# Kernel tuning notes

Hardware: AMD Instinct MI355X
Metric: run time of the kernel (lower is better)

The kernel has to match this reference:

```python
import jax, jax.numpy as jnp
import numpy as np

N_EMBD = 1024
N_HEAD = 16


def setup_inputs() -> dict:
    key = jax.random.key(0)
    ks = jax.random.split(key, 5)
    C = N_EMBD
    x = jax.random.normal(ks[0], (4, 2048, C), dtype=jnp.float32)
    s = 1.0 / np.sqrt(C)
    W_attn = jax.random.normal(ks[1], (C, 3 * C), dtype=jnp.float32) * s
    b_attn = jnp.zeros((3 * C,), dtype=jnp.float32)
    W_proj = jax.random.normal(ks[2], (C, C), dtype=jnp.float32) * s
    b_proj = jnp.zeros((C,), dtype=jnp.float32)
    return {"x": x, "W_attn": W_attn, "b_attn": b_attn, "W_proj": W_proj, "b_proj": b_proj}


def reference(x, W_attn, b_attn, W_proj, b_proj):
    B, T, C = x.shape
    H = N_HEAD
    D = C // H
    qkv = x @ W_attn + b_attn                      # [B,T,3C]
    q, k, v = jnp.split(qkv, 3, axis=-1)
    # [B,H,T,D]
    q = q.reshape(B, T, H, D).transpose(0, 2, 1, 3)
    k = k.reshape(B, T, H, D).transpose(0, 2, 1, 3)
    v = v.reshape(B, T, H, D).transpose(0, 2, 1, 3)
    scale = 1.0 / jnp.sqrt(jnp.asarray(D, dtype=x.dtype))
    att = jnp.einsum('bhqd,bhkd->bhqk', q, k) * scale   # [B,H,T,T]
    causal = jnp.tril(jnp.ones((T, T), dtype=bool))
    att = jnp.where(causal, att, jnp.finfo(att.dtype).min)
    att = jax.nn.softmax(att, axis=-1)
    y = jnp.einsum('bhqk,bhkd->bhqd', att, v)            # [B,H,T,D]
    y = y.transpose(0, 2, 1, 3).reshape(B, T, C)
    return y @ W_proj + b_proj
```

## Files before the change

### kernel.cpp

```cpp
#include <hip/hip_runtime.h>
#include <type_traits>

typedef __attribute__((ext_vector_type(8))) short short8;
typedef __attribute__((ext_vector_type(8))) unsigned short ushort8;
typedef __attribute__((ext_vector_type(4))) float floatx4;

__device__ __forceinline__ unsigned short f2bf(float f) {
    union { float f; unsigned int i; } v;
    v.f = f;
    unsigned int u = v.i;
    unsigned int r = (u + 0x7FFFu + ((u >> 16) & 1u)) >> 16;
    return (unsigned short)r;
}

__device__ __forceinline__ void gload_lds16(const unsigned short* g, unsigned short* lds_base) {
    __builtin_amdgcn_global_load_lds(
        (const __attribute__((address_space(1))) unsigned int*)g,
        (__attribute__((address_space(3))) unsigned int*)lds_base,
        16, 0, 0);
}

__global__ __launch_bounds__(256) void cvt_f32_bf16_kernel(
    const float* __restrict__ src, unsigned short* __restrict__ dst, int n8)
{
    int i = blockIdx.x * 256 + threadIdx.x;
    if (i >= n8) return;
    const float4* s = (const float4*)src + (size_t)i * 2;
    float4 a = s[0];
    float4 b = s[1];
    ushort8 r;
    r[0] = f2bf(a.x); r[1] = f2bf(a.y); r[2] = f2bf(a.z); r[3] = f2bf(a.w);
    r[4] = f2bf(b.x); r[5] = f2bf(b.y); r[6] = f2bf(b.z); r[7] = f2bf(b.w);
    *((ushort8*)dst + i) = r;
}

__global__ __launch_bounds__(256) void transpose_cvt_kernel(
    const float* __restrict__ src, unsigned short* __restrict__ dst, int K, int N)
{
    __shared__ float tile[32][33];
    const int tx = threadIdx.x & 31;
    const int ty = threadIdx.x >> 5;
    const int k0 = blockIdx.y * 32, n0 = blockIdx.x * 32;
#pragma unroll
    for (int i = 0; i < 4; ++i)
        tile[ty + i * 8][tx] = src[(size_t)(k0 + ty + i * 8) * N + n0 + tx];
    __syncthreads();
#pragma unroll
    for (int i = 0; i < 4; ++i)
        dst[(size_t)(n0 + ty + i * 8) * K + k0 + tx] = f2bf(tile[tx][ty + i * 8]);
}

template <int MODE, typename OutT>
__global__ __launch_bounds__(256) void gemm128_kernel(
    const unsigned short* __restrict__ A,
    const unsigned short* __restrict__ Bt,
    const float* __restrict__ bias,
    OutT* __restrict__ C,
    unsigned short* __restrict__ Qo,
    unsigned short* __restrict__ Ko,
    unsigned short* __restrict__ Vto,
    int M, int N, int K)
{
    __shared__ __align__(16) unsigned short As[128 * 32];
    __shared__ __align__(16) unsigned short Bs[128 * 32];

    const int tid  = threadIdx.x;
    const int lane = tid & 63;
    const int w    = tid >> 6;
    const int wm   = w & 1;
    const int wn   = w >> 1;
    const int quad = lane >> 4;
    const int l16  = lane & 15;

    const int m0 = blockIdx.y * 128;
    const int n0 = blockIdx.x * 128;

    floatx4 acc[4][4];
#pragma unroll
    for (int i = 0; i < 4; ++i)
#pragma unroll
        for (int j = 0; j < 4; ++j) acc[i][j] = (floatx4)0.0f;

    const int r0 = tid >> 2;
    const int kc = (tid & 3) << 3;
    const unsigned short* Ag = A  + (size_t)(m0 + r0) * K + kc;
    const unsigned short* Bg = Bt + (size_t)(n0 + r0) * K + kc;
    unsigned short* AsW = As + w * 512;
    unsigned short* BsW = Bs + w * 512;

    for (int k0 = 0; k0 < K; k0 += 32) {
        __syncthreads();
#pragma unroll
        for (int i = 0; i < 2; ++i) {
            gload_lds16(Ag + (size_t)(i * 64) * K + k0, AsW + i * 2048);
            gload_lds16(Bg + (size_t)(i * 64) * K + k0, BsW + i * 2048);
        }
        __syncthreads();

        short8 a[4], b[4];
#pragma unroll
        for (int mi = 0; mi < 4; ++mi)
            a[mi] = *(const short8*)&As[(wm * 64 + mi * 16 + l16) * 32 + (quad << 3)];
#pragma unroll
        for (int ni = 0; ni < 4; ++ni)
            b[ni] = *(const short8*)&Bs[(wn * 64 + ni * 16 + l16) * 32 + (quad << 3)];
#pragma unroll
        for (int mi = 0; mi < 4; ++mi)
#pragma unroll
            for (int ni = 0; ni < 4; ++ni)
                acc[mi][ni] = __builtin_amdgcn_mfma_f32_16x16x32_bf16(a[mi], b[ni], acc[mi][ni], 0, 0, 0);
    }

#pragma unroll
    for (int ni = 0; ni < 4; ++ni) {
        const int n = n0 + wn * 64 + ni * 16 + l16;
        const float bval = bias[n];
#pragma unroll
        for (int mi = 0; mi < 4; ++mi) {
#pragma unroll
            for (int r = 0; r < 4; ++r) {
                const int m = m0 + wm * 64 + mi * 16 + (quad << 2) + r;
                const float val = acc[mi][ni][r] + bval;
                if constexpr (MODE == 0) {
                    if constexpr (std::is_same<OutT, unsigned short>::value)
                        C[(size_t)m * N + n] = f2bf(val);
                    else
                        C[(size_t)m * N + n] = val;
                } else {
                    const int seg = n >> 10;
                    const int nl  = n & 1023;
                    if (seg == 0) {
                        Qo[(size_t)m * 1024 + nl] = f2bf(val);
                    } else if (seg == 1) {
                        Ko[(size_t)m * 1024 + nl] = f2bf(val);
                    } else {
                        const int bb = m >> 11, t = m & 2047;
                        Vto[((size_t)bb * 1024 + nl) * 2048 + t] = f2bf(val);
                    }
                }
            }
        }
    }
}

__global__ __launch_bounds__(256) void attn_kernel(
    const unsigned short* __restrict__ Q,
    const unsigned short* __restrict__ Kq,
    const unsigned short* __restrict__ Vt,
    unsigned short* __restrict__ Y)
{
    const int T = 2048;

    int idx = blockIdx.x;
    int qt  = 31 - (idx >> 6);
    int bh  = idx & 63;
    int b   = bh >> 4;
    int h   = bh & 15;

    const int tid  = threadIdx.x;
    const int lane = tid & 63;
    const int w    = tid >> 6;
    const int quad = lane >> 4;
    const int l16  = lane & 15;

    __shared__ __align__(16) unsigned short Ks[32][72];
    __shared__ __align__(16) unsigned short Vs[64 * 32];
    __shared__ __align__(16) unsigned short Ps[4][16][40];

    const unsigned short* qp =
        Q + (size_t)(b * T + qt * 64 + (w << 4) + l16) * 1024 + h * 64;
    short8 qf0 = *(const short8*)(qp + (quad << 3));
    short8 qf1 = *(const short8*)(qp + 32 + (quad << 3));

    float l_i[4];
    floatx4 o[4];
#pragma unroll
    for (int r = 0; r < 4; ++r) l_i[r] = 0.0f;
#pragma unroll
    for (int ns = 0; ns < 4; ++ns) o[ns] = (floatx4)0.0f;

    const int srow = tid >> 3;
    const int scol = (tid & 7) << 3;
    const int vrow = tid >> 2;
    const int vcol = (tid & 3) << 3;
    const unsigned short* vbase = Vt + ((size_t)(b * 1024 + h * 64 + vrow)) * 2048 + vcol;
    const int qrow  = qt * 64 + (w << 4) + (quad << 2);
    const int wrow0 = qt * 64 + (w << 4);

    const float SC = 0.125f;
    const float MB = -12.0f;

    const int ktiles = 2 * qt + 2;
    for (int kt = 0; kt < ktiles; ++kt) {
        const int key0 = kt << 5;
        __syncthreads();
        const unsigned short* kp =
            Kq + (size_t)(b * T + key0 + srow) * 1024 + h * 64 + scol;
        *(int4*)&Ks[srow][scol] = *(const int4*)kp;
        gload_lds16(vbase + key0, Vs + w * 512);
        __syncthreads();

        floatx4 s0 = (floatx4)0.0f, s1 = (floatx4)0.0f;
        {
            short8 kf00 = *(const short8*)&Ks[l16][quad << 3];
            short8 kf01 = *(const short8*)&Ks[l16][32 + (quad << 3)];
            short8 kf10 = *(const short8*)&Ks[16 + l16][quad << 3];
            short8 kf11 = *(const short8*)&Ks[16 + l16][32 + (quad << 3)];
            s0 = __builtin_amdgcn_mfma_f32_16x16x32_bf16(qf0, kf00, s0, 0, 0, 0);
            s0 = __builtin_amdgcn_mfma_f32_16x16x32_bf16(qf1, kf01, s0, 0, 0, 0);
            s1 = __builtin_amdgcn_mfma_f32_16x16x32_bf16(qf0, kf10, s1, 0, 0, 0);
            s1 = __builtin_amdgcn_mfma_f32_16x16x32_bf16(qf1, kf11, s1, 0, 0, 0);
        }

        if (key0 + 31 <= wrow0) {
#pragma unroll
            for (int r = 0; r < 4; ++r) {
                float p0 = __expf(fmaf(s0[r], SC, MB));
                float p1 = __expf(fmaf(s1[r], SC, MB));
                l_i[r] += p0 + p1;
                Ps[w][(quad << 2) + r][l16]      = f2bf(p0);
                Ps[w][(quad << 2) + r][16 + l16] = f2bf(p1);
            }
        } else {
            const int kg0 = key0 + l16;
#pragma unroll
            for (int r = 0; r < 4; ++r) {
                float a0 = (kg0      <= qrow + r) ? fmaf(s0[r], SC, MB) : -1e5f;
                float a1 = (kg0 + 16 <= qrow + r) ? fmaf(s1[r], SC, MB) : -1e5f;
                float p0 = __expf(a0);
                float p1 = __expf(a1);
                l_i[r] += p0 + p1;
                Ps[w][(quad << 2) + r][l16]      = f2bf(p0);
                Ps[w][(quad << 2) + r][16 + l16] = f2bf(p1);
            }
        }

        short8 pf = *(const short8*)&Ps[w][l16][quad << 3];
#pragma unroll
        for (int ns = 0; ns < 4; ++ns) {
            short8 vf = *(const short8*)&Vs[((ns << 4) + l16) * 32 + (quad << 3)];
            o[ns] = __builtin_amdgcn_mfma_f32_16x16x32_bf16(pf, vf, o[ns], 0, 0, 0);
        }
    }

#pragma unroll
    for (int r = 0; r < 4; ++r) {
        float s = l_i[r];
        s += __shfl_xor(s, 1, 64);
        s += __shfl_xor(s, 2, 64);
        s += __shfl_xor(s, 4, 64);
        s += __shfl_xor(s, 8, 64);
        l_i[r] = 1.0f / s;
    }

#pragma unroll
    for (int ns = 0; ns < 4; ++ns) {
        int d = (ns << 4) + l16;
#pragma unroll
        for (int r = 0; r < 4; ++r) {
            int t = qt * 64 + (w << 4) + (quad << 2) + r;
            Y[(size_t)(b * T + t) * 1024 + h * 64 + d] = f2bf(o[ns][r] * l_i[r]);
        }
    }
}

extern "C" void kernel_launch(void* const* d_in, const int* in_sizes, int n_in,
                              void* d_out, int out_size, void* d_ws, size_t ws_size,
                              hipStream_t stream) {
    const float* x  = (const float*)d_in[0];
    const float* Wa = (const float*)d_in[1];
    const float* ba = (const float*)d_in[2];
    const float* Wp = (const float*)d_in[3];
    const float* bp = (const float*)d_in[4];
    float* out = (float*)d_out;

    const size_t NX = (size_t)8192 * 1024;

    unsigned short* Qb  = (unsigned short*)d_ws;
    unsigned short* Kb  = Qb  + NX;
    unsigned short* Vtb = Kb  + NX;
    unsigned short* Yb  = Vtb + NX;
    unsigned short* xb  = Yb  + NX;
    unsigned short* Wat = xb  + NX;
    unsigned short* Wpt = Wat + (size_t)3072 * 1024;

    cvt_f32_bf16_kernel<<<(int)(NX / 8 / 256), 256, 0, stream>>>(x, xb, (int)(NX / 8));
    transpose_cvt_kernel<<<dim3(3072 / 32, 1024 / 32), 256, 0, stream>>>(Wa, Wat, 1024, 3072);
    transpose_cvt_kernel<<<dim3(1024 / 32, 1024 / 32), 256, 0, stream>>>(Wp, Wpt, 1024, 1024);

    gemm128_kernel<1, unsigned short><<<dim3(3072 / 128, 8192 / 128), 256, 0, stream>>>(
        xb, Wat, ba, (unsigned short*)nullptr, Qb, Kb, Vtb, 8192, 3072, 1024);

    attn_kernel<<<4 * 16 * (2048 / 64), 256, 0, stream>>>(Qb, Kb, Vtb, Yb);

    gemm128_kernel<0, float><<<dim3(1024 / 128, 8192 / 128), 256, 0, stream>>>(
        Yb, Wpt, bp, out, nullptr, nullptr, nullptr, 8192, 1024, 1024);
}
```

Measured before the change: 293.5 us.

## Widen attention key tiles to 64 with direct-to-LDS K/V loads; vectorize V^T stores

The attention kernel now processes 64 keys per iteration instead of 32. That halves the loop trips and barrier pairs and doubles the MFMA work per synchronization. K and V tiles are both loaded with global_load_lds into a k-chunk-major LDS layout, replacing register-staged K stores. The QKV GEMM epilogue writes the transposed V as packed 4-element 8-byte stores instead of scattered 2-byte stores. The costs are more LDS and registers per block and coarser causal masking on the diagonal tile.

Measured after the change: 276.0 us. 6.0% less time.

```diff
diff --git a/kernel.cpp b/kernel.cpp
--- a/kernel.cpp
+++ b/kernel.cpp
@@ -115,28 +115,37 @@
     for (int ni = 0; ni < 4; ++ni) {
         const int n = n0 + wn * 64 + ni * 16 + l16;
         const float bval = bias[n];
+        const int seg = n >> 10;
+        const int nl  = n & 1023;
 #pragma unroll
         for (int mi = 0; mi < 4; ++mi) {
-#pragma unroll
-            for (int r = 0; r < 4; ++r) {
-                const int m = m0 + wm * 64 + mi * 16 + (quad << 2) + r;
-                const float val = acc[mi][ni][r] + bval;
-                if constexpr (MODE == 0) {
+            if constexpr (MODE == 0) {
+#pragma unroll
+                for (int r = 0; r < 4; ++r) {
+                    const int m = m0 + wm * 64 + mi * 16 + (quad << 2) + r;
+                    const float val = acc[mi][ni][r] + bval;
                     if constexpr (std::is_same<OutT, unsigned short>::value)
                         C[(size_t)m * N + n] = f2bf(val);
                     else
                         C[(size_t)m * N + n] = val;
+                }
+            } else {
+                if (seg < 2) {
+                    unsigned short* P = (seg == 0) ? Qo : Ko;
+#pragma unroll
+                    for (int r = 0; r < 4; ++r) {
+                        const int m = m0 + wm * 64 + mi * 16 + (quad << 2) + r;
+                        P[(size_t)m * 1024 + nl] = f2bf(acc[mi][ni][r] + bval);
+                    }
                 } else {
-                    const int seg = n >> 10;
-                    const int nl  = n & 1023;
-                    if (seg == 0) {
-                        Qo[(size_t)m * 1024 + nl] = f2bf(val);
-                    } else if (seg == 1) {
-                        Ko[(size_t)m * 1024 + nl] = f2bf(val);
-                    } else {
-                        const int bb = m >> 11, t = m & 2047;
-                        Vto[((size_t)bb * 1024 + nl) * 2048 + t] = f2bf(val);
-                    }
+                    const int mb = m0 + wm * 64 + mi * 16 + (quad << 2);
+                    const int bb = mb >> 11, t0 = mb & 2047;
+                    unsigned int lo = (unsigned int)f2bf(acc[mi][ni][0] + bval) |
+                                      ((unsigned int)f2bf(acc[mi][ni][1] + bval) << 16);
+                    unsigned int hi = (unsigned int)f2bf(acc[mi][ni][2] + bval) |
+                                      ((unsigned int)f2bf(acc[mi][ni][3] + bval) << 16);
+                    uint2 pv; pv.x = lo; pv.y = hi;
+                    *(uint2*)(Vto + ((size_t)bb * 1024 + nl) * 2048 + t0) = pv;
                 }
             }
         }
@@ -163,9 +172,9 @@
     const int quad = lane >> 4;
     const int l16  = lane & 15;
 
-    __shared__ __align__(16) unsigned short Ks[32][72];
-    __shared__ __align__(16) unsigned short Vs[64 * 32];
-    __shared__ __align__(16) unsigned short Ps[4][16][40];
+    __shared__ __align__(16) unsigned short Ks2[8 * 64 * 8];
+    __shared__ __align__(16) unsigned short Vs2[8 * 64 * 8];
+    __shared__ __align__(16) unsigned short Ps[4][16][72];
 
     const unsigned short* qp =
         Q + (size_t)(b * T + qt * 64 + (w << 4) + l16) * 1024 + h * 64;
@@ -179,78 +188,83 @@
 #pragma unroll
     for (int ns = 0; ns < 4; ++ns) o[ns] = (floatx4)0.0f;
 
-    const int srow = tid >> 3;
-    const int scol = (tid & 7) << 3;
-    const int vrow = tid >> 2;
-    const int vcol = (tid & 3) << 3;
-    const unsigned short* vbase = Vt + ((size_t)(b * 1024 + h * 64 + vrow)) * 2048 + vcol;
+    const unsigned short* kg0p = Kq + (size_t)(b * T + lane) * 1024 + h * 64 + (w) * 8;
+    const unsigned short* kg1p = Kq + (size_t)(b * T + lane) * 1024 + h * 64 + (w + 4) * 8;
+    const unsigned short* vg0p = Vt + ((size_t)(b * 1024 + h * 64 + lane)) * 2048 + (w) * 8;
+    const unsigned short* vg1p = Vt + ((size_t)(b * 1024 + h * 64 + lane)) * 2048 + (w + 4) * 8;
+
     const int qrow  = qt * 64 + (w << 4) + (quad << 2);
-    const int wrow0 = qt * 64 + (w << 4);
 
     const float SC = 0.125f;
     const float MB = -12.0f;
 
-    const int ktiles = 2 * qt + 2;
+    const int ktiles = qt + 1;
     for (int kt = 0; kt < ktiles; ++kt) {
-        const int key0 = kt << 5;
+        const int key0 = kt << 6;
         __syncthreads();
-        const unsigned short* kp =
-            Kq + (size_t)(b * T + key0 + srow) * 1024 + h * 64 + scol;
-        *(int4*)&Ks[srow][scol] = *(const int4*)kp;
-        gload_lds16(vbase + key0, Vs + w * 512);
+        gload_lds16(kg0p + (size_t)key0 * 1024, Ks2 + (w) * 512);
+        gload_lds16(kg1p + (size_t)key0 * 1024, Ks2 + (w + 4) * 512);
+        gload_lds16(vg0p + key0, Vs2 + (w) * 512);
+        gload_lds16(vg1p + key0, Vs2 + (w + 4) * 512);
         __syncthreads();
 
-        floatx4 s0 = (floatx4)0.0f, s1 = (floatx4)0.0f;
-        {
-            short8 kf00 = *(const short8*)&Ks[l16][quad << 3];
-            short8 kf01 = *(const short8*)&Ks[l16][32 + (quad << 3)];
-            short8 kf10 = *(const short8*)&Ks[16 + l16][quad << 3];
-            short8 kf11 = *(const short8*)&Ks[16 + l16][32 + (quad << 3)];
-            s0 = __builtin_amdgcn_mfma_f32_16x16x32_bf16(qf0, kf00, s0, 0, 0, 0);
-            s0 = __builtin_amdgcn_mfma_f32_16x16x32_bf16(qf1, kf01, s0, 0, 0, 0);
-            s1 = __builtin_amdgcn_mfma_f32_16x16x32_bf16(qf0, kf10, s1, 0, 0, 0);
-            s1 = __builtin_amdgcn_mfma_f32_16x16x32_bf16(qf1, kf11, s1, 0, 0, 0);
-        }
-
-        if (key0 + 31 <= wrow0) {
+        floatx4 s[4];
+#pragma unroll
+        for (int ks = 0; ks < 4; ++ks) {
+            s[ks] = (floatx4)0.0f;
+            short8 kf0 = *(const short8*)&Ks2[((0 * 4 + quad) * 64 + ks * 16 + l16) * 8];
+            short8 kf1 = *(const short8*)&Ks2[((1 * 4 + quad) * 64 + ks * 16 + l16) * 8];
+            s[ks] = __builtin_amdgcn_mfma_f32_16x16x32_bf16(qf0, kf0, s[ks], 0, 0, 0);
+            s[ks] = __builtin_amdgcn_mfma_f32_16x16x32_bf16(qf1, kf1, s[ks], 0, 0, 0);
+        }
+
+        if (kt < qt) {
 #pragma unroll
             for (int r = 0; r < 4; ++r) {
-                float p0 = __expf(fmaf(s0[r], SC, MB));
-                float p1 = __expf(fmaf(s1[r], SC, MB));
-                l_i[r] += p0 + p1;
-                Ps[w][(quad << 2) + r][l16]      = f2bf(p0);
-                Ps[w][(quad << 2) + r][16 + l16] = f2bf(p1);
+                float lsum = 0.0f;
+#pragma unroll
+                for (int ks = 0; ks < 4; ++ks) {
+                    float p = __expf(fmaf(s[ks][r], SC, MB));
+                    lsum += p;
+                    Ps[w][(quad << 2) + r][ks * 16 + l16] = f2bf(p);
+                }
+                l_i[r] += lsum;
             }
         } else {
-            const int kg0 = key0 + l16;
+            const int kg = key0 + l16;
 #pragma unroll
             for (int r = 0; r < 4; ++r) {
-                float a0 = (kg0      <= qrow + r) ? fmaf(s0[r], SC, MB) : -1e5f;
-                float a1 = (kg0 + 16 <= qrow + r) ? fmaf(s1[r], SC, MB) : -1e5f;
-                float p0 = __expf(a0);
-                float p1 = __expf(a1);
-                l_i[r] += p0 + p1;
-                Ps[w][(quad << 2) + r][l16]      = f2bf(p0);
-                Ps[w][(quad << 2) + r][16 + l16] = f2bf(p1);
+                float lsum = 0.0f;
+#pragma unroll
+                for (int ks = 0; ks < 4; ++ks) {
+                    float a = (kg + ks * 16 <= qrow + r) ? fmaf(s[ks][r], SC, MB) : -1e5f;
+                    float p = __expf(a);
+                    lsum += p;
+                    Ps[w][(quad << 2) + r][ks * 16 + l16] = f2bf(p);
+                }
+                l_i[r] += lsum;
             }
         }
 
-        short8 pf = *(const short8*)&Ps[w][l16][quad << 3];
+        short8 pf0 = *(const short8*)&Ps[w][l16][quad << 3];
+        short8 pf1 = *(const short8*)&Ps[w][l16][32 + (quad << 3)];
 #pragma unroll
         for (int ns = 0; ns < 4; ++ns) {
-            short8 vf = *(const short8*)&Vs[((ns << 4) + l16) * 32 + (quad << 3)];
-            o[ns] = __builtin_amdgcn_mfma_f32_16x16x32_bf16(pf, vf, o[ns], 0, 0, 0);
+            short8 vf0 = *(const short8*)&Vs2[((0 * 4 + quad) * 64 + ns * 16 + l16) * 8];
+            short8 vf1 = *(const short8*)&Vs2[((1 * 4 + quad) * 64 + ns * 16 + l16) * 8];
+            o[ns] = __builtin_amdgcn_mfma_f32_16x16x32_bf16(pf0, vf0, o[ns], 0, 0, 0);
+            o[ns] = __builtin_amdgcn_mfma_f32_16x16x32_bf16(pf1, vf1, o[ns], 0, 0, 0);
         }
     }
 
 #pragma unroll
     for (int r = 0; r < 4; ++r) {
-        float s = l_i[r];
-        s += __shfl_xor(s, 1, 64);
-        s += __shfl_xor(s, 2, 64);
-        s += __shfl_xor(s, 4, 64);
-        s += __shfl_xor(s, 8, 64);
-        l_i[r] = 1.0f / s;
+        float ssum = l_i[r];
+        ssum += __shfl_xor(ssum, 1, 64);
+        ssum += __shfl_xor(ssum, 2, 64);
+        ssum += __shfl_xor(ssum, 4, 64);
+        ssum += __shfl_xor(ssum, 8, 64);
+        l_i[r] = 1.0f / ssum;
     }
 
 #pragma unroll
```
